# Kernel tuning notes

Hardware: AMD Instinct MI355X
Metric: run time of the kernel (lower is better)

Reference implementation:

```python
import jax, jax.numpy as jnp
import numpy as np
import math

N_EMBD = 1024
N_HEAD = 16
BLOCK_SIZE = 2048
B, T = 2, 2048


def setup_inputs() -> dict:
    key = jax.random.key(0)
    ks = jax.random.split(key, 12)
    s = 0.02
    C = N_EMBD
    return {
        "x": jax.random.normal(ks[0], (B, T, C), dtype=jnp.float32),
        # LayerNorm 1
        "ln1_w": jnp.ones((C,), jnp.float32),
        "ln1_b": jnp.zeros((C,), jnp.float32),
        # attention: weights stored [in, out]
        "attn_w": jax.random.normal(ks[1], (C, 3 * C), dtype=jnp.float32) * s,
        "attn_b": jnp.zeros((3 * C,), jnp.float32),
        "proj_w": jax.random.normal(ks[2], (C, C), dtype=jnp.float32) * s,
        "proj_b": jnp.zeros((C,), jnp.float32),
        # LayerNorm 2
        "ln2_w": jnp.ones((C,), jnp.float32),
        "ln2_b": jnp.zeros((C,), jnp.float32),
        # MLP
        "fc_w": jax.random.normal(ks[3], (C, 4 * C), dtype=jnp.float32) * s,
        "fc_b": jnp.zeros((4 * C,), jnp.float32),
        "mlp_proj_w": jax.random.normal(ks[4], (4 * C, C), dtype=jnp.float32) * s,
        "mlp_proj_b": jnp.zeros((C,), jnp.float32),
    }


def _layernorm(x, w, b, eps=1e-5):
    mu = jnp.mean(x, axis=-1, keepdims=True)
    var = jnp.mean(jnp.square(x - mu), axis=-1, keepdims=True)
    return (x - mu) * jax.lax.rsqrt(var + eps) * w + b


def _attention(x, attn_w, attn_b, proj_w, proj_b):
    Bn, Tn, C = x.shape
    hs = C // N_HEAD
    qkv = x @ attn_w + attn_b                      # [B,T,3C]
    q, k, v = jnp.split(qkv, 3, axis=-1)
    # [B,H,T,hs]
    q = q.reshape(Bn, Tn, N_HEAD, hs).transpose(0, 2, 1, 3)
    k = k.reshape(Bn, Tn, N_HEAD, hs).transpose(0, 2, 1, 3)
    v = v.reshape(Bn, Tn, N_HEAD, hs).transpose(0, 2, 1, 3)
    att = jnp.einsum('bhqd,bhkd->bhqk', q, k) / math.sqrt(hs)  # [B,H,T,T]
    mask = jnp.tril(jnp.ones((Tn, Tn), dtype=bool))
    att = jnp.where(mask, att, -jnp.inf)
    att = jax.nn.softmax(att, axis=-1)
    y = jnp.einsum('bhqk,bhkd->bhqd', att, v)      # [B,H,T,hs]
    y = y.transpose(0, 2, 1, 3).reshape(Bn, Tn, C)
    return y @ proj_w + proj_b


def reference(x, ln1_w, ln1_b, attn_w, attn_b, proj_w, proj_b,
              ln2_w, ln2_b, fc_w, fc_b, mlp_proj_w, mlp_proj_b):
    x = x + _attention(_layernorm(x, ln1_w, ln1_b), attn_w, attn_b, proj_w, proj_b)
    h = _layernorm(x, ln2_w, ln2_b)
    h = jax.nn.gelu(h @ fc_w + fc_b, approximate=False)  # torch nn.GELU default = exact erf
    return x + (h @ mlp_proj_w + mlp_proj_b)
```

## Files before the change

### kernel.cpp

```cpp
#include <hip/hip_runtime.h>
#include <math.h>

typedef short s8x __attribute__((ext_vector_type(8)));
typedef float f32x4 __attribute__((ext_vector_type(4)));
typedef int   i32x2 __attribute__((ext_vector_type(2)));

__device__ __forceinline__ float bf2f(short u) {
    return __uint_as_float(((unsigned int)(unsigned short)u) << 16);
}
__device__ __forceinline__ short f2bf(float f) {
    unsigned int x = __float_as_uint(f);
    unsigned int r = (x + 0x7FFFu + ((x >> 16) & 1u)) >> 16;
    return (short)(unsigned short)r;
}

__device__ __forceinline__ void gl2lds16(const short* g, const short* l) {
    __builtin_amdgcn_global_load_lds(
        (const __attribute__((address_space(1))) void*)(unsigned long long)g,
        (__attribute__((address_space(3))) void*)(unsigned int)(unsigned long long)l,
        16, 0, 0);
}

__device__ __forceinline__ void ln_row(const float* __restrict__ xin,
                                       const float* __restrict__ w,
                                       const float* __restrict__ bb,
                                       short* __restrict__ out, int row, int lane) {
    const float4* xr = (const float4*)(xin + (long)row * 1024);
    float4 v[4];
    float s1 = 0.f, s2 = 0.f;
#pragma unroll
    for (int i = 0; i < 4; ++i) {
        v[i] = xr[lane + i * 64];
        s1 += v[i].x + v[i].y + v[i].z + v[i].w;
        s2 += v[i].x*v[i].x + v[i].y*v[i].y + v[i].z*v[i].z + v[i].w*v[i].w;
    }
#pragma unroll
    for (int off = 32; off > 0; off >>= 1) {
        s1 += __shfl_xor(s1, off, 64);
        s2 += __shfl_xor(s2, off, 64);
    }
    const float mu = s1 * (1.0f / 1024.0f);
    float var = s2 * (1.0f / 1024.0f) - mu * mu;
    var = fmaxf(var, 0.0f);
    const float rs = rsqrtf(var + 1e-5f);
    short4* orow = (short4*)(out + (long)row * 1024);
#pragma unroll
    for (int i = 0; i < 4; ++i) {
        const int ci = (lane + i * 64) * 4;
        const float4 wv = *(const float4*)(w + ci);
        const float4 bv = *(const float4*)(bb + ci);
        short4 o;
        o.x = f2bf((v[i].x - mu) * rs * wv.x + bv.x);
        o.y = f2bf((v[i].y - mu) * rs * wv.y + bv.y);
        o.z = f2bf((v[i].z - mu) * rs * wv.z + bv.z);
        o.w = f2bf((v[i].w - mu) * rs * wv.w + bv.w);
        orow[lane + i * 64] = o;
    }
}

__global__ __launch_bounds__(256) void ln_k(const float* __restrict__ xin,
                                            const float* __restrict__ w,
                                            const float* __restrict__ bb,
                                            short* __restrict__ out) {
    ln_row(xin, w, bb, out, blockIdx.x * 4 + (threadIdx.x >> 6), threadIdx.x & 63);
}

__global__ __launch_bounds__(256) void pre_k(
        const float* __restrict__ w0, const float* __restrict__ w1,
        const float* __restrict__ w2, const float* __restrict__ w3,
        short* __restrict__ o0, short* __restrict__ o1,
        short* __restrict__ o2, short* __restrict__ o3,
        const float* __restrict__ x, const float* __restrict__ ln1w,
        const float* __restrict__ ln1b, short* __restrict__ xln) {
    int bid = blockIdx.x;
    if (bid >= 12288) {
        ln_row(x, ln1w, ln1b, xln, (bid - 12288) * 4 + (threadIdx.x >> 6), threadIdx.x & 63);
        return;
    }
    const float* in; short* out; int K, N, nx;
    if (bid < 3072)      { in = w0; out = o0; K = 1024; N = 3072; nx = 96; }
    else if (bid < 4096) { bid -= 3072; in = w1; out = o1; K = 1024; N = 1024; nx = 32; }
    else if (bid < 8192) { bid -= 4096; in = w2; out = o2; K = 1024; N = 4096; nx = 128; }
    else                 { bid -= 8192; in = w3; out = o3; K = 4096; N = 1024; nx = 32; }
    const int n0 = (bid % nx) * 32, k0 = (bid / nx) * 32;
    __shared__ float tile[32][33];
    const int tx = threadIdx.x & 31, ty = threadIdx.x >> 5;
#pragma unroll
    for (int i = 0; i < 4; ++i) {
        const int k = ty + i * 8;
        tile[k][tx] = in[(long)(k0 + k) * N + n0 + tx];
    }
    __syncthreads();
#pragma unroll
    for (int i = 0; i < 4; ++i) {
        const int n = ty + i * 8;
        out[(long)(n0 + n) * K + k0 + tx] = f2bf(tile[tx][n]);
    }
}

template <int EPI, typename OutT>
__device__ __forceinline__ void epi_store(OutT* out, const float* resid, long oidx, float v) {
    if constexpr (EPI == 0) {
        out[oidx] = f2bf(v);
    } else if constexpr (EPI == 1) {
        const float u = v * (0.79788456080f + 0.03567740814f * v * v);
        v = v / (1.0f + __expf(-2.0f * u));
        out[oidx] = f2bf(v);
    } else {
        v += resid[oidx];
        out[oidx] = v;
    }
}

template <int EPI, typename OutT>
__global__ __launch_bounds__(256) void gemm_k(const short* __restrict__ A,
                                              const short* __restrict__ Bt,
                                              const float* __restrict__ bias,
                                              const float* __restrict__ resid,
                                              OutT* __restrict__ out,
                                              int M, int N, int K) {
    __shared__ __align__(16) short sA[2][128 * 32];
    __shared__ __align__(16) short sB[2][128 * 32];
    const int tid = threadIdx.x;
    const int lane = tid & 63, wave = tid >> 6;
    const int wr = (wave >> 1) * 64, wc = (wave & 1) * 64;
    const int lrow = lane & 15, quad = lane >> 4;
    const int bm = blockIdx.y * 128, bn = blockIdx.x * 128;
    const short* Ap = A + (long)(bm + (tid >> 2)) * K + (tid & 3) * 8;
    const short* Bp = Bt + (long)(bn + (tid >> 2)) * K + (tid & 3) * 8;
    const long rowstep = (long)64 * K;

    auto stage = [&](int p, int k0) {
        gl2lds16(Ap + k0,           sA[p] + tid * 8);
        gl2lds16(Ap + rowstep + k0, sA[p] + 2048 + tid * 8);
        gl2lds16(Bp + k0,           sB[p] + tid * 8);
        gl2lds16(Bp + rowstep + k0, sB[p] + 2048 + tid * 8);
    };

    f32x4 acc[4][4] = {};
    stage(0, 0);
    const int S = K >> 5;
    for (int s = 0; s < S; ++s) {
        const int p = s & 1;
        __syncthreads();
        if (s + 1 < S) stage(p ^ 1, (s + 1) << 5);
        const short* pA = sA[p];
        const short* pB = sB[p];
        s8x af[4], bfr[4];
#pragma unroll
        for (int i = 0; i < 4; ++i) af[i]  = *(const s8x*)(pA + (wr + i*16 + lrow) * 32 + quad * 8);
#pragma unroll
        for (int j = 0; j < 4; ++j) bfr[j] = *(const s8x*)(pB + (wc + j*16 + lrow) * 32 + quad * 8);
#pragma unroll
        for (int i = 0; i < 4; ++i)
#pragma unroll
            for (int j = 0; j < 4; ++j)
                acc[i][j] = __builtin_amdgcn_mfma_f32_16x16x32_bf16(af[i], bfr[j], acc[i][j], 0, 0, 0);
    }
#pragma unroll
    for (int i = 0; i < 4; ++i) {
#pragma unroll
        for (int j = 0; j < 4; ++j) {
#pragma unroll
            for (int r = 0; r < 4; ++r) {
                const int row = bm + wr + i*16 + quad*4 + r;
                const int col = bn + wc + j*16 + lrow;
                epi_store<EPI>(out, resid, (long)row * N + col, acc[i][j][r] + bias[col]);
            }
        }
    }
}

template <int EPI, typename OutT>
__global__ __launch_bounds__(256) void gemm64_k(const short* __restrict__ A,
                                                const short* __restrict__ Bt,
                                                const float* __restrict__ bias,
                                                const float* __restrict__ resid,
                                                OutT* __restrict__ out,
                                                int M, int N, int K) {
    __shared__ __align__(16) short sA[2][2][64 * 32];
    __shared__ __align__(16) short sB[2][2][128 * 32];
    const int tid = threadIdx.x;
    const int lane = tid & 63, wave = tid >> 6;
    const int lrow = lane & 15, quad = lane >> 4;
    const int bm = blockIdx.y * 64, bn = blockIdx.x * 128;
    const short* Ap = A + (long)(bm + (tid >> 2)) * K + (tid & 3) * 8;
    const short* Bp = Bt + (long)(bn + (tid >> 2)) * K + (tid & 3) * 8;
    const long rowstep = (long)64 * K;

    auto stage = [&](int p, int k0) {
#pragma unroll
        for (int hp = 0; hp < 2; ++hp) {
            gl2lds16(Ap + k0 + hp * 32,           sA[p][hp] + tid * 8);
            gl2lds16(Bp + k0 + hp * 32,           sB[p][hp] + tid * 8);
            gl2lds16(Bp + rowstep + k0 + hp * 32, sB[p][hp] + 2048 + tid * 8);
        }
    };

    f32x4 acc[8] = {};
    stage(0, 0);
    const int S = K >> 6;
    for (int s = 0; s < S; ++s) {
        const int p = s & 1;
        __syncthreads();
        if (s + 1 < S) stage(p ^ 1, (s + 1) << 6);
#pragma unroll
        for (int hp = 0; hp < 2; ++hp) {
            const s8x af = *(const s8x*)(sA[p][hp] + (wave * 16 + lrow) * 32 + quad * 8);
#pragma unroll
            for (int j = 0; j < 8; ++j) {
                const s8x bf = *(const s8x*)(sB[p][hp] + (j * 16 + lrow) * 32 + quad * 8);
                acc[j] = __builtin_amdgcn_mfma_f32_16x16x32_bf16(af, bf, acc[j], 0, 0, 0);
            }
        }
    }
#pragma unroll
    for (int j = 0; j < 8; ++j) {
#pragma unroll
        for (int r = 0; r < 4; ++r) {
            const int row = bm + wave * 16 + quad * 4 + r;
            const int col = bn + j * 16 + lrow;
            epi_store<EPI>(out, resid, (long)row * N + col, acc[j][r] + bias[col]);
        }
    }
}

#define ATT_CS (0.125f * 1.4426950408889634f)
#define ATT_C0 (14.426950408889634f)

#define TR16(dst, off) \
    asm volatile("ds_read_b64_tr_b16 %0, %1 offset:" off : "=v"(dst) : "v"(tva))

__global__ __launch_bounds__(256) void attn_k(const short* __restrict__ qkv,
                                              short* __restrict__ y) {
    const int bx = blockIdx.x;
    const int b = blockIdx.y >> 4, h = blockIdx.y & 15;
    const int qtA = bx, qtB = 31 - bx;
    const int tid = threadIdx.x, lane = tid & 63, wave = tid >> 6;
    const int lrow = lane & 15, quad = lane >> 4;
    const long base = (long)b * 2048 * 3072;

    __shared__ __align__(16) short sK[2][64 * 64];
    __shared__ __align__(16) short sV[2][4096];

    s8x qfA0, qfA1, qfB0, qfB1;
    {
        const short* qpA = qkv + base + (long)(qtA * 64 + wave * 16 + lrow) * 3072 + h * 64 + quad * 8;
        qfA0 = *(const s8x*)qpA; qfA1 = *(const s8x*)(qpA + 32);
        const short* qpB = qkv + base + (long)(qtB * 64 + wave * 16 + lrow) * 3072 + h * 64 + quad * 8;
        qfB0 = *(const s8x*)qpB; qfB1 = *(const s8x*)(qpB + 32);
    }
    f32x4 oA[4], oB[4];
    float lA = 0.f, lB = 0.f;
#pragma unroll
    for (int d = 0; d < 4; ++d) { oA[d] = f32x4{0.f,0.f,0.f,0.f}; oB[d] = f32x4{0.f,0.f,0.f,0.f}; }

    const int srow = tid >> 3, sg = tid & 7;
    const int sw0 = ((srow & 7) ^ (srow >> 3)) & 7;
    const int sw1 = (((srow + 32) & 7) ^ ((srow + 32) >> 3)) & 7;
    const short* kbase = qkv + base + 1024 + h * 64;
    auto issueK = [&](int p, int k0) {
        gl2lds16(kbase + (long)(k0 + srow) * 3072      + (sg ^ sw0) * 8, sK[p] + tid * 8);
        gl2lds16(kbase + (long)(k0 + srow + 32) * 3072 + (sg ^ sw1) * 8, sK[p] + 2048 + tid * 8);
    };

    const int vslot   = (tid >> 3) & 7;
    const int vkbl    = 2 * (vslot & 3) + (vslot >> 2);
    const int vklocal = vkbl * 4 + ((tid >> 1) & 3);
    const short* vsrc = qkv + base + 2048 + h * 64
                      + (long)vklocal * 3072 + wave * 16 + 8 * (tid & 1);
    auto issueV = [&](int p, int k0) {
        gl2lds16(vsrc + (long)k0 * 3072,        sV[p] + tid * 8);
        gl2lds16(vsrc + (long)(k0 + 32) * 3072, sV[p] + 2048 + tid * 8);
    };
    const unsigned trb = (unsigned)(unsigned long long)(&sV[0][0]) + (unsigned)lane * 8u;

    auto tile_step = [&](const s8x& qf0, const s8x& qf1, const s8x* kf0, const s8x* kf1,
                         const s8x (*vfr)[4], f32x4* o, float& lsum, int qt, int kt, int k0) {
        f32x4 s[4];
#pragma unroll
        for (int ct = 0; ct < 4; ++ct) {
            f32x4 t = f32x4{0.f, 0.f, 0.f, 0.f};
            t = __builtin_amdgcn_mfma_f32_16x16x32_bf16(kf0[ct], qf0, t, 0, 0, 0);
            t = __builtin_amdgcn_mfma_f32_16x16x32_bf16(kf1[ct], qf1, t, 0, 0, 0);
            s[ct] = t;
        }
        const int qrow = qt * 64 + wave * 16 + lrow;
        float pv[4][4];
        if (kt == qt) {
#pragma unroll
            for (int ct = 0; ct < 4; ++ct)
#pragma unroll
                for (int r = 0; r < 4; ++r) {
                    const int key = k0 + ct * 16 + quad * 4 + r;
                    const float pp = exp2f(fmaf(s[ct][r], ATT_CS, -ATT_C0));
                    const float pt = __uint_as_float(__float_as_uint(pp) & 0xFFFF0000u);
                    pv[ct][r] = (key > qrow) ? 0.f : pt;
                }
        } else {
#pragma unroll
            for (int ct = 0; ct < 4; ++ct)
#pragma unroll
                for (int r = 0; r < 4; ++r) {
                    const float pp = exp2f(fmaf(s[ct][r], ATT_CS, -ATT_C0));
                    pv[ct][r] = __uint_as_float(__float_as_uint(pp) & 0xFFFF0000u);
                }
        }
#pragma unroll
        for (int ct = 0; ct < 4; ++ct)
            lsum += (pv[ct][0] + pv[ct][1]) + (pv[ct][2] + pv[ct][3]);

        unsigned int w2[4][2];
#pragma unroll
        for (int ct = 0; ct < 4; ++ct)
#pragma unroll
            for (int p2 = 0; p2 < 2; ++p2)
                w2[ct][p2] = __builtin_amdgcn_perm(__float_as_uint(pv[ct][2 * p2 + 1]),
                                                   __float_as_uint(pv[ct][2 * p2]), 0x07060302u);
        s8x pa[2];
#pragma unroll
        for (int ks = 0; ks < 2; ++ks) {
            auto rAC = __builtin_amdgcn_permlane32_swap((int)w2[2 * ks][0], (int)w2[2 * ks + 1][0], false, false);
            auto rBD = __builtin_amdgcn_permlane32_swap((int)w2[2 * ks][1], (int)w2[2 * ks + 1][1], false, false);
            auto mAC = __builtin_amdgcn_permlane16_swap(rAC[0], rAC[1], false, false);
            auto mBD = __builtin_amdgcn_permlane16_swap(rBD[0], rBD[1], false, false);
            int4 f;
            f.x = mAC[0]; f.y = mBD[0]; f.z = mAC[1]; f.w = mBD[1];
            pa[ks] = *(const s8x*)&f;
        }
#pragma unroll
        for (int ks = 0; ks < 2; ++ks)
#pragma unroll
            for (int dt = 0; dt < 4; ++dt)
                o[dt] = __builtin_amdgcn_mfma_f32_16x16x32_bf16(pa[ks], vfr[ks][dt], o[dt], 0, 0, 0);
    };

    issueK(0, 0);
    issueV(0, 0);
    for (int kt = 0; kt <= qtB; ++kt) {
        const int p = kt & 1, k0 = kt * 64;
        __syncthreads();
        if (kt < qtB) { issueK(p ^ 1, k0 + 64); issueV(p ^ 1, k0 + 64); }

        s8x kf0[4], kf1[4];
#pragma unroll
        for (int ct = 0; ct < 4; ++ct) {
            const int row = ct * 16 + lrow;
            const int swr = ((row & 7) ^ (row >> 3)) & 7;
            kf0[ct] = *(const s8x*)(sK[p] + row * 64 + ((quad ^ swr) * 8));
            kf1[ct] = *(const s8x*)(sK[p] + row * 64 + (((4 + quad) ^ swr) * 8));
        }

        const unsigned tva = trb + (unsigned)(p << 13);
        i32x2 tr[16];
        TR16(tr[0],  "0");    TR16(tr[1],  "512");
        TR16(tr[2],  "1024"); TR16(tr[3],  "1536");
        TR16(tr[4],  "2048"); TR16(tr[5],  "2560");
        TR16(tr[6],  "3072"); TR16(tr[7],  "3584");
        TR16(tr[8],  "4096"); TR16(tr[9],  "4608");
        TR16(tr[10], "5120"); TR16(tr[11], "5632");
        TR16(tr[12], "6144"); TR16(tr[13], "6656");
        TR16(tr[14], "7168"); TR16(tr[15], "7680");
        asm volatile("s_waitcnt lgkmcnt(0)" ::: "memory");
        __builtin_amdgcn_sched_barrier(0);
        s8x vfr[2][4];
#pragma unroll
        for (int ks = 0; ks < 2; ++ks)
#pragma unroll
            for (int dt = 0; dt < 4; ++dt) {
                const int i2 = ks * 8 + dt * 2;
                int4 f;
                f.x = tr[i2][0]; f.y = tr[i2][1];
                f.z = tr[i2 + 1][0]; f.w = tr[i2 + 1][1];
                vfr[ks][dt] = *(const s8x*)&f;
            }

        if (kt <= qtA) tile_step(qfA0, qfA1, kf0, kf1, vfr, oA, lA, qtA, kt, k0);
        tile_step(qfB0, qfB1, kf0, kf1, vfr, oB, lB, qtB, kt, k0);
    }

    lA += __shfl_xor(lA, 16, 64); lA += __shfl_xor(lA, 32, 64);
    lB += __shfl_xor(lB, 16, 64); lB += __shfl_xor(lB, 32, 64);
    float rA[4], rB[4];
#pragma unroll
    for (int r = 0; r < 4; ++r) {
        rA[r] = 1.0f / __shfl(lA, quad * 4 + r, 64);
        rB[r] = 1.0f / __shfl(lB, quad * 4 + r, 64);
    }
#pragma unroll
    for (int dt = 0; dt < 4; ++dt) {
#pragma unroll
        for (int r = 0; r < 4; ++r) {
            const int qA = qtA * 64 + wave * 16 + quad * 4 + r;
            const int qB = qtB * 64 + wave * 16 + quad * 4 + r;
            y[((long)b * 2048 + qA) * 1024 + h * 64 + dt * 16 + lrow] = f2bf(oA[dt][r] * rA[r]);
            y[((long)b * 2048 + qB) * 1024 + h * 64 + dt * 16 + lrow] = f2bf(oB[dt][r] * rB[r]);
        }
    }
}

extern "C" void kernel_launch(void* const* d_in, const int* in_sizes, int n_in,
                              void* d_out, int out_size, void* d_ws, size_t ws_size,
                              hipStream_t stream) {
    const float* x      = (const float*)d_in[0];
    const float* ln1_w  = (const float*)d_in[1];
    const float* ln1_b  = (const float*)d_in[2];
    const float* attn_w = (const float*)d_in[3];
    const float* attn_b = (const float*)d_in[4];
    const float* proj_w = (const float*)d_in[5];
    const float* proj_b = (const float*)d_in[6];
    const float* ln2_w  = (const float*)d_in[7];
    const float* ln2_b  = (const float*)d_in[8];
    const float* fc_w   = (const float*)d_in[9];
    const float* fc_b   = (const float*)d_in[10];
    const float* mlp_w  = (const float*)d_in[11];
    const float* mlp_b  = (const float*)d_in[12];

    char* ws = (char*)d_ws;
    short* attn_wt = (short*)(ws + 0);
    short* proj_wt = (short*)(ws + 6291456L);
    short* fc_wt   = (short*)(ws + 8388608L);
    short* mlp_wt  = (short*)(ws + 16777216L);
    short* slotA   = (short*)(ws + 25165824L);
    short* slotB   = (short*)(ws + 33554432L);

    short* xln  = slotA;
    short* yb   = slotA;
    short* hb   = slotA;
    short* qkvb = slotB;
    short* hh   = slotB;
    float* x1   = (float*)d_out;
    float* outp = (float*)d_out;

    pre_k<<<13312, 256, 0, stream>>>(attn_w, proj_w, fc_w, mlp_w,
                                     attn_wt, proj_wt, fc_wt, mlp_wt,
                                     x, ln1_w, ln1_b, xln);

    gemm_k<0, short><<<dim3(24, 32), 256, 0, stream>>>(xln, attn_wt, attn_b, nullptr, qkvb, 4096, 3072, 1024);
    attn_k<<<dim3(16, 32), 256, 0, stream>>>(qkvb, yb);
    gemm64_k<2, float><<<dim3(8, 64), 256, 0, stream>>>(yb, proj_wt, proj_b, x, x1, 4096, 1024, 1024);
    ln_k<<<1024, 256, 0, stream>>>(x1, ln2_w, ln2_b, hb);
    gemm_k<1, short><<<dim3(32, 32), 256, 0, stream>>>(hb, fc_wt, fc_b, nullptr, hh, 4096, 4096, 1024);
    gemm64_k<3, float><<<dim3(8, 64), 256, 0, stream>>>(hh, mlp_wt, mlp_b, x1, outp, 4096, 1024, 4096);
}
```

Measured before the change: 332.6 us.

## Keep next-stage global-to-LDS loads in flight across barriers with partial vmcnt waits

The two GEMM kernels and the attention kernel now prefetch the first two stages up front. In the loop, each stage waits only on the older stage's loads using s_waitcnt vmcnt(n), followed by a raw s_barrier, instead of a full __syncthreads. The freed buffer is refilled after a second barrier at the end of each iteration, so one stage of global loads overlaps the current MFMA work. This adds an extra barrier per iteration and depends on the hardcoded vmcnt counts matching the number of loads each stage issues.

Result: no change. 335.6 us (+0.9%).

```diff
diff --git a/kernel.cpp b/kernel.cpp
--- a/kernel.cpp
+++ b/kernel.cpp
@@ -20,6 +20,13 @@
         (__attribute__((address_space(3))) void*)(unsigned int)(unsigned long long)l,
         16, 0, 0);
 }
+
+__device__ __forceinline__ void block_sync() {
+    asm volatile("" ::: "memory");
+    __builtin_amdgcn_s_barrier();
+    asm volatile("" ::: "memory");
+}
+#define WAITV(n) asm volatile("s_waitcnt vmcnt(" #n ")" ::: "memory")
 
 __device__ __forceinline__ void ln_row(const float* __restrict__ xin,
                                        const float* __restrict__ w,
@@ -138,12 +145,13 @@
     };
 
     f32x4 acc[4][4] = {};
+    const int S = K >> 5;
     stage(0, 0);
-    const int S = K >> 5;
+    stage(1, 32);
     for (int s = 0; s < S; ++s) {
         const int p = s & 1;
-        __syncthreads();
-        if (s + 1 < S) stage(p ^ 1, (s + 1) << 5);
+        if (s + 1 < S) { WAITV(4); } else { WAITV(0); }
+        block_sync();
         const short* pA = sA[p];
         const short* pB = sB[p];
         s8x af[4], bfr[4];
@@ -156,6 +164,8 @@
 #pragma unroll
             for (int j = 0; j < 4; ++j)
                 acc[i][j] = __builtin_amdgcn_mfma_f32_16x16x32_bf16(af[i], bfr[j], acc[i][j], 0, 0, 0);
+        block_sync();
+        if (s + 2 < S) stage(p, (s + 2) << 5);
     }
 #pragma unroll
     for (int i = 0; i < 4; ++i) {
@@ -198,12 +208,13 @@
     };
 
     f32x4 acc[8] = {};
+    const int S = K >> 6;
     stage(0, 0);
-    const int S = K >> 6;
+    stage(1, 64);
     for (int s = 0; s < S; ++s) {
         const int p = s & 1;
-        __syncthreads();
-        if (s + 1 < S) stage(p ^ 1, (s + 1) << 6);
+        if (s + 1 < S) { WAITV(6); } else { WAITV(0); }
+        block_sync();
 #pragma unroll
         for (int hp = 0; hp < 2; ++hp) {
             const s8x af = *(const s8x*)(sA[p][hp] + (wave * 16 + lrow) * 32 + quad * 8);
@@ -213,6 +224,8 @@
                 acc[j] = __builtin_amdgcn_mfma_f32_16x16x32_bf16(af, bf, acc[j], 0, 0, 0);
             }
         }
+        block_sync();
+        if (s + 2 < S) stage(p, (s + 2) << 6);
     }
 #pragma unroll
     for (int j = 0; j < 8; ++j) {
@@ -335,12 +348,12 @@
                 o[dt] = __builtin_amdgcn_mfma_f32_16x16x32_bf16(pa[ks], vfr[ks][dt], o[dt], 0, 0, 0);
     };
 
-    issueK(0, 0);
-    issueV(0, 0);
+    issueK(0, 0);  issueV(0, 0);
+    issueK(1, 64); issueV(1, 64);
     for (int kt = 0; kt <= qtB; ++kt) {
         const int p = kt & 1, k0 = kt * 64;
-        __syncthreads();
-        if (kt < qtB) { issueK(p ^ 1, k0 + 64); issueV(p ^ 1, k0 + 64); }
+        if (kt < qtB) { WAITV(4); } else { WAITV(0); }
+        block_sync();
 
         s8x kf0[4], kf1[4];
 #pragma unroll
@@ -377,6 +390,9 @@
 
         if (kt <= qtA) tile_step(qfA0, qfA1, kf0, kf1, vfr, oA, lA, qtA, kt, k0);
         tile_step(qfB0, qfB1, kf0, kf1, vfr, oB, lB, qtB, kt, k0);
+
+        block_sync();
+        if (kt + 2 <= qtB) { issueK(p, k0 + 128); issueV(p, k0 + 128); }
     }
 
     lA += __shfl_xor(lA, 16, 64); lA += __shfl_xor(lA, 32, 64);
```
